# Performance work log

Measured on AMD Instinct MI355X. Metric: run time of the kernel, lower is better.

## Reference

```python
import jax, jax.numpy as jnp
import numpy as np

N_NODES = 50000
N_EDGES = 800000
HID = 128
LAYERS = 3


def setup_inputs() -> dict:
    key = jax.random.key(0)
    k1, k2, k3, k4 = jax.random.split(key, 4)
    x = jax.random.normal(k1, (N_NODES, HID), dtype=jnp.float32)
    edge_index = jax.random.randint(k2, (2, N_EDGES), 0, N_NODES, dtype=jnp.int64)
    # Glorot-ish scale so 3 stacked layers stay numerically tame
    Ws = jax.random.normal(k3, (LAYERS, HID, HID), dtype=jnp.float32) * (1.0 / np.sqrt(HID))
    bs = jax.random.normal(k4, (LAYERS, HID), dtype=jnp.float32) * 0.01
    return {"x": x, "edge_index": edge_index, "Ws": Ws, "bs": bs}


def reference(x, edge_index, Ws, bs):
    """Stacked GCNConv (add_self_loops=False): out = D^-1/2 A D^-1/2 (x W) + b.
    Returns (final_x, embeddings_list) like the torch module."""
    N = x.shape[0]
    src = edge_index[0]  # message sources (x_j)
    dst = edge_index[1]  # aggregation targets
    # gcn_norm with unit edge weights, no self loops: in-degree on targets
    deg = jax.ops.segment_sum(jnp.ones(src.shape[0], dtype=x.dtype), dst, num_segments=N)
    dinv = jnp.where(deg > 0, jax.lax.rsqrt(jnp.maximum(deg, 1.0)), 0.0).astype(x.dtype)
    norm = dinv[src] * dinv[dst]  # [E]

    embeddings = [x]
    for l in range(Ws.shape[0]):
        h = x @ Ws[l]                               # [N, D] dense transform
        msg = h[src] * norm[:, None]                # [E, D] gather + normalize
        x = jax.ops.segment_sum(msg, dst, num_segments=N) + bs[l]  # scatter-add
        embeddings.append(x)
    return (x, embeddings)
```

## Files before the change

### kernel.cpp

```cpp
#include <hip/hip_runtime.h>

#define N_NODES 50000
#define N_EDGES 800000
#define HID 128
#define SLOT (N_NODES * HID)
#define W_STRIDE (HID * HID)

#define OFF_CNT    0ul
#define OFF_DINV   200192ul
#define OFF_RPTR   400384ul
#define OFF_RFILL  600576ul
#define OFF_BSUM   800768ul
#define OFF_BOFS   801280ul
#define OFF_SRCS   801792ul
#define OFF_H_WS   4001792ul


__global__ void k_zero_cnt(int* __restrict__ cnt) {
    int i = blockIdx.x * blockDim.x + threadIdx.x;
    if (i < N_NODES) cnt[i] = 0;
}

__global__ void k_count(const int* __restrict__ ei, int* __restrict__ cnt) {
    int e = blockIdx.x * blockDim.x + threadIdx.x;
    if (e < N_EDGES) {
        int d = ei[N_EDGES + e];
        atomicAdd(&cnt[d], 1);
    }
}

__global__ void k_scan_block(const int* __restrict__ cnt, int* __restrict__ rptr,
                             int* __restrict__ bsum) {
    __shared__ int s[512];
    int tid = threadIdx.x;
    int gid = blockIdx.x * 512 + tid;
    int v = (gid < N_NODES) ? cnt[gid] : 0;
    s[tid] = v;
    __syncthreads();
    for (int off = 1; off < 512; off <<= 1) {
        int t = (tid >= off) ? s[tid - off] : 0;
        __syncthreads();
        s[tid] += t;
        __syncthreads();
    }
    if (gid < N_NODES) rptr[gid] = s[tid] - v;
    if (tid == 511) bsum[blockIdx.x] = s[511];
}

__global__ void k_scan_sums(const int* __restrict__ bsum, int* __restrict__ bofs, int nb) {
    __shared__ int s[128];
    int tid = threadIdx.x;
    int v = (tid < nb) ? bsum[tid] : 0;
    s[tid] = v;
    __syncthreads();
    for (int off = 1; off < 128; off <<= 1) {
        int t = (tid >= off) ? s[tid - off] : 0;
        __syncthreads();
        s[tid] += t;
        __syncthreads();
    }
    if (tid < nb) bofs[tid] = s[tid] - v;
}

__global__ void k_scan_add(int* __restrict__ rptr, int* __restrict__ rfill,
                           const int* __restrict__ bofs, const int* __restrict__ cnt,
                           float* __restrict__ dinv) {
    int gid = blockIdx.x * blockDim.x + threadIdx.x;
    if (gid < N_NODES) {
        int r = rptr[gid] + bofs[gid >> 9];
        rptr[gid] = r;
        rfill[gid] = r;
        int c = cnt[gid];
        dinv[gid] = (c > 0) ? rsqrtf((float)c) : 0.0f;
    }
    if (gid == 0) rptr[N_NODES] = N_EDGES;
}

__global__ void k_scatter(const int* __restrict__ ei, int* __restrict__ rfill,
                          int* __restrict__ srcs) {
    int e = blockIdx.x * blockDim.x + threadIdx.x;
    if (e < N_EDGES) {
        int sv = ei[e];
        int d  = ei[N_EDGES + e];
        int pos = atomicAdd(&rfill[d], 1);
        srcs[pos] = sv;
    }
}

__launch_bounds__(256, 2)
__global__ void k_gemm_scale(const float* __restrict__ X, const float* __restrict__ W,
                             const float* __restrict__ dinv, float* __restrict__ H) {
    __shared__ float sW[HID * 64];
    __shared__ float sX[64 * HID];
    int tid   = threadIdx.x;
    int chalf = blockIdx.x & 1;
    int row0  = (blockIdx.x >> 1) * 64;

    const float4* W4  = (const float4*)W;
    float4*       sW4 = (float4*)sW;
    for (int j = tid; j < 2048; j += 256) {
        int k  = j >> 4;
        int c4 = j & 15;
        sW4[j] = W4[k * 32 + chalf * 16 + c4];
    }

    const float4* X4  = (const float4*)X;
    float4*       sX4 = (float4*)sX;
    for (int j = tid; j < 2048; j += 256) {
        int r   = j >> 5;
        int c4  = j & 31;
        int row = row0 + r;
        float4 v = {0.f, 0.f, 0.f, 0.f};
        if (row < N_NODES) v = X4[row * 32 + c4];
        sX4[r * 32 + (c4 ^ ((r >> 3) & 7))] = v;
    }
    __syncthreads();

    int ty  = tid >> 4;
    int tx  = tid & 15;
    int swz = (ty >> 1) & 7;

    float4 acc[4];
    #pragma unroll
    for (int r = 0; r < 4; ++r) acc[r] = {0.f, 0.f, 0.f, 0.f};

    #pragma unroll 4
    for (int k0 = 0; k0 < HID; k0 += 4) {
        int k4 = k0 >> 2;
        float4 wv[4];
        #pragma unroll
        for (int kk = 0; kk < 4; ++kk)
            wv[kk] = sW4[(k0 + kk) * 16 + tx];
        float4 xv[4];
        #pragma unroll
        for (int r = 0; r < 4; ++r)
            xv[r] = sX4[(ty * 4 + r) * 32 + (k4 ^ swz)];
        #pragma unroll
        for (int r = 0; r < 4; ++r) {
            float xk0 = xv[r].x, xk1 = xv[r].y, xk2 = xv[r].z, xk3 = xv[r].w;
            acc[r].x += xk0 * wv[0].x + xk1 * wv[1].x + xk2 * wv[2].x + xk3 * wv[3].x;
            acc[r].y += xk0 * wv[0].y + xk1 * wv[1].y + xk2 * wv[2].y + xk3 * wv[3].y;
            acc[r].z += xk0 * wv[0].z + xk1 * wv[1].z + xk2 * wv[2].z + xk3 * wv[3].z;
            acc[r].w += xk0 * wv[0].w + xk1 * wv[1].w + xk2 * wv[2].w + xk3 * wv[3].w;
        }
    }

    float4* H4 = (float4*)H;
    #pragma unroll
    for (int r = 0; r < 4; ++r) {
        int row = row0 + ty * 4 + r;
        if (row < N_NODES) {
            float dv = dinv[row];
            float4 o = acc[r];
            o.x *= dv; o.y *= dv; o.z *= dv; o.w *= dv;
            H4[row * 32 + chalf * 16 + tx] = o;
        }
    }
}

__global__ void k_agg(const float* __restrict__ H, const int* __restrict__ rptr,
                      const int* __restrict__ srcs, const float* __restrict__ dinv,
                      const float* __restrict__ bias, float* __restrict__ out0,
                      float* __restrict__ out1) {
    int wid  = (blockIdx.x * blockDim.x + threadIdx.x) >> 6;
    int lane = threadIdx.x & 63;
    if (wid >= N_NODES) return;
    int half = lane >> 5;
    int l32  = lane & 31;

    int beg = rptr[wid];
    int end = rptr[wid + 1];
    int deg = end - beg;

    const float4* H4 = (const float4*)H;

    float4 a0 = {0.f,0.f,0.f,0.f}, a1 = {0.f,0.f,0.f,0.f};
    float4 a2 = {0.f,0.f,0.f,0.f}, a3 = {0.f,0.f,0.f,0.f};

    int p = beg;
    int n8 = beg + (deg & ~7);
    for (; p < n8; p += 8) {
        int base = p + half * 4;
        int s0 = srcs[base + 0];
        int s1 = srcs[base + 1];
        int s2 = srcs[base + 2];
        int s3 = srcs[base + 3];
        float4 h0 = H4[s0 * 32 + l32];
        float4 h1 = H4[s1 * 32 + l32];
        float4 h2 = H4[s2 * 32 + l32];
        float4 h3 = H4[s3 * 32 + l32];
        a0.x += h0.x; a0.y += h0.y; a0.z += h0.z; a0.w += h0.w;
        a1.x += h1.x; a1.y += h1.y; a1.z += h1.z; a1.w += h1.w;
        a2.x += h2.x; a2.y += h2.y; a2.z += h2.z; a2.w += h2.w;
        a3.x += h3.x; a3.y += h3.y; a3.z += h3.z; a3.w += h3.w;
    }
    int rem   = deg & 7;
    int pairs = rem >> 1;
    for (int i = 0; i < pairs; ++i) {
        int e = p + 2 * i + half;
        float4 hv = H4[srcs[e] * 32 + l32];
        if (i == 0)      { a0.x += hv.x; a0.y += hv.y; a0.z += hv.z; a0.w += hv.w; }
        else if (i == 1) { a1.x += hv.x; a1.y += hv.y; a1.z += hv.z; a1.w += hv.w; }
        else             { a2.x += hv.x; a2.y += hv.y; a2.z += hv.z; a2.w += hv.w; }
    }
    if (rem & 1) {
        float4 hv = H4[srcs[end - 1] * 32 + l32];
        if (half == 0) { a3.x += hv.x; a3.y += hv.y; a3.z += hv.z; a3.w += hv.w; }
    }

    float4 s;
    s.x = a0.x + a1.x + a2.x + a3.x;
    s.y = a0.y + a1.y + a2.y + a3.y;
    s.z = a0.z + a1.z + a2.z + a3.z;
    s.w = a0.w + a1.w + a2.w + a3.w;
    s.x += __shfl_xor(s.x, 32);
    s.y += __shfl_xor(s.y, 32);
    s.z += __shfl_xor(s.z, 32);
    s.w += __shfl_xor(s.w, 32);

    if (half == 0) {
        float dv  = dinv[wid];
        float4 bb = ((const float4*)bias)[l32];
        float4 res;
        res.x = s.x * dv + bb.x;
        res.y = s.y * dv + bb.y;
        res.z = s.z * dv + bb.z;
        res.w = s.w * dv + bb.w;
        ((float4*)out0)[wid * 32 + l32] = res;
        if (out1) ((float4*)out1)[wid * 32 + l32] = res;
    }
}

__global__ void k_copy(const float* __restrict__ src, float* __restrict__ dst, int n4) {
    int i = blockIdx.x * blockDim.x + threadIdx.x;
    if (i < n4) ((float4*)dst)[i] = ((const float4*)src)[i];
}


extern "C" void kernel_launch(void* const* d_in, const int* in_sizes, int n_in,
                              void* d_out, int out_size, void* d_ws, size_t ws_size,
                              hipStream_t stream) {
    const float* x  = (const float*)d_in[0];
    const int*   ei = (const int*)d_in[1];
    const float* Ws = (const float*)d_in[2];
    const float* bs = (const float*)d_in[3];
    float* out = (float*)d_out;
    char*  ws  = (char*)d_ws;

    int*   cnt   = (int*)  (ws + OFF_CNT);
    float* dinv  = (float*)(ws + OFF_DINV);
    int*   rptr  = (int*)  (ws + OFF_RPTR);
    int*   rfill = (int*)  (ws + OFF_RFILL);
    int*   bsum  = (int*)  (ws + OFF_BSUM);
    int*   bofs  = (int*)  (ws + OFF_BOFS);
    int*   srcs  = (int*)  (ws + OFF_SRCS);

    float* slot0 = out;
    float* slot1 = out + 1l * SLOT;
    float* slot2 = out + 2l * SLOT;
    float* slot3 = out + 3l * SLOT;
    float* slot4 = out + 4l * SLOT;

    bool   h_in_ws = ws_size >= (size_t)(OFF_H_WS + (size_t)SLOT * 4);
    float* h = h_in_ws ? (float*)(ws + OFF_H_WS) : slot0;

    const int NB_NODE = (N_NODES + 255) / 256;
    const int NB_EDGE = (N_EDGES + 255) / 256;
    const int NB_SCAN = (N_NODES + 511) / 512;

    k_zero_cnt  <<<NB_NODE, 256, 0, stream>>>(cnt);
    k_count     <<<NB_EDGE, 256, 0, stream>>>(ei, cnt);
    k_scan_block<<<NB_SCAN, 512, 0, stream>>>(cnt, rptr, bsum);
    k_scan_sums <<<1, 128, 0, stream>>>(bsum, bofs, NB_SCAN);
    k_scan_add  <<<NB_NODE, 256, 0, stream>>>(rptr, rfill, bofs, cnt, dinv);
    k_scatter   <<<NB_EDGE, 256, 0, stream>>>(ei, rfill, srcs);

    k_copy<<<SLOT / 4 / 256, 256, 0, stream>>>(x, slot1, SLOT / 4);

    const int NB_GEMM = 2 * ((N_NODES + 63) / 64);
    const int NB_AGG  = (N_NODES + 3) / 4;

    k_gemm_scale<<<NB_GEMM, 256, 0, stream>>>(x, Ws + 0 * W_STRIDE, dinv, h);
    k_agg       <<<NB_AGG, 256, 0, stream>>>(h, rptr, srcs, dinv, bs + 0 * HID, slot2, nullptr);

    k_gemm_scale<<<NB_GEMM, 256, 0, stream>>>(slot2, Ws + 1 * W_STRIDE, dinv, h);
    k_agg       <<<NB_AGG, 256, 0, stream>>>(h, rptr, srcs, dinv, bs + 1 * HID, slot3, nullptr);

    k_gemm_scale<<<NB_GEMM, 256, 0, stream>>>(slot3, Ws + 2 * W_STRIDE, dinv, h);
    if (h_in_ws) {
        k_agg<<<NB_AGG, 256, 0, stream>>>(h, rptr, srcs, dinv, bs + 2 * HID, slot4, slot0);
    } else {
        k_agg<<<NB_AGG, 256, 0, stream>>>(h, rptr, srcs, dinv, bs + 2 * HID, slot4, nullptr);
        k_copy<<<SLOT / 4 / 256, 256, 0, stream>>>(slot4, slot0, SLOT / 4);
    }
}
```

Before: 399.9 us.

## Fuse CSR preprocessing and input copy into one cooperative kernel

Replaces the six preprocessing launches (zero, count, block scan, sum scan, scan add, scatter) plus the input copy with a single cooperative kernel that uses grid-wide syncs between phases. The x-to-slot1 copy overlaps with the degree counting phase. This removes per-launch overhead and idle gaps between the small kernels, at the cost of grid.sync barriers and a fixed 1024-block grid. If the cooperative launch fails, it falls back to the original multi-kernel path.

```diff
diff --git a/kernel.cpp b/kernel.cpp
--- a/kernel.cpp
+++ b/kernel.cpp
@@ -1,4 +1,7 @@
 #include <hip/hip_runtime.h>
+#include <hip/hip_cooperative_groups.h>
+
+namespace cg = cooperative_groups;
 
 #define N_NODES 50000
 #define N_EDGES 800000
@@ -11,9 +14,86 @@
 #define OFF_RPTR   400384ul
 #define OFF_RFILL  600576ul
 #define OFF_BSUM   800768ul
-#define OFF_BOFS   801280ul
-#define OFF_SRCS   801792ul
-#define OFF_H_WS   4001792ul
+#define OFF_BOFS   801792ul
+#define OFF_SRCS   802816ul
+#define OFF_H_WS   4002816ul
+
+__global__ void __launch_bounds__(256, 8)
+k_preproc(const int* __restrict__ ei, const float* __restrict__ x,
+          float* __restrict__ slot1, int* __restrict__ cnt,
+          float* __restrict__ dinv, int* __restrict__ rptr,
+          int* __restrict__ rfill, int* __restrict__ bsum,
+          int* __restrict__ bofs, int* __restrict__ srcs) {
+    cg::grid_group grid = cg::this_grid();
+    const int tid = threadIdx.x;
+    const int bid = blockIdx.x;
+    const int nb  = gridDim.x;
+    const int gstride = nb * 256;
+    const int g = bid * 256 + tid;
+    const int NCHUNK = (N_NODES + 255) / 256;
+
+    __shared__ int sc[256];
+
+    for (int i = g; i < N_NODES; i += gstride) cnt[i] = 0;
+    grid.sync();
+
+    for (int e = g; e < N_EDGES; e += gstride)
+        atomicAdd(&cnt[ei[N_EDGES + e]], 1);
+    {
+        const float4* x4  = (const float4*)x;
+        float4*       s14 = (float4*)slot1;
+        for (int i = g; i < SLOT / 4; i += gstride) s14[i] = x4[i];
+    }
+    grid.sync();
+
+    for (int c = bid; c < NCHUNK; c += nb) {
+        int idx = c * 256 + tid;
+        int v = (idx < N_NODES) ? cnt[idx] : 0;
+        sc[tid] = v;
+        __syncthreads();
+        for (int off = 1; off < 256; off <<= 1) {
+            int t = (tid >= off) ? sc[tid - off] : 0;
+            __syncthreads();
+            sc[tid] += t;
+            __syncthreads();
+        }
+        if (idx < N_NODES) rptr[idx] = sc[tid] - v;
+        if (tid == 255) bsum[c] = sc[255];
+        __syncthreads();
+    }
+    grid.sync();
+
+    if (bid == 0) {
+        int v = (tid < NCHUNK) ? bsum[tid] : 0;
+        sc[tid] = v;
+        __syncthreads();
+        for (int off = 1; off < 256; off <<= 1) {
+            int t = (tid >= off) ? sc[tid - off] : 0;
+            __syncthreads();
+            sc[tid] += t;
+            __syncthreads();
+        }
+        if (tid < NCHUNK) bofs[tid] = sc[tid] - v;
+    }
+    grid.sync();
+
+    for (int i = g; i < N_NODES; i += gstride) {
+        int r = rptr[i] + bofs[i >> 8];
+        rptr[i]  = r;
+        rfill[i] = r;
+        int c = cnt[i];
+        dinv[i] = (c > 0) ? rsqrtf((float)c) : 0.0f;
+    }
+    if (g == 0) rptr[N_NODES] = N_EDGES;
+    grid.sync();
+
+    for (int e = g; e < N_EDGES; e += gstride) {
+        int sv = ei[e];
+        int d  = ei[N_EDGES + e];
+        int pos = atomicAdd(&rfill[d], 1);
+        srcs[pos] = sv;
+    }
+}
 
 
 __global__ void k_zero_cnt(int* __restrict__ cnt) {
@@ -23,10 +103,7 @@
 
 __global__ void k_count(const int* __restrict__ ei, int* __restrict__ cnt) {
     int e = blockIdx.x * blockDim.x + threadIdx.x;
-    if (e < N_EDGES) {
-        int d = ei[N_EDGES + e];
-        atomicAdd(&cnt[d], 1);
-    }
+    if (e < N_EDGES) atomicAdd(&cnt[ei[N_EDGES + e]], 1);
 }
 
 __global__ void k_scan_block(const int* __restrict__ cnt, int* __restrict__ rptr,
@@ -85,6 +162,11 @@
         int pos = atomicAdd(&rfill[d], 1);
         srcs[pos] = sv;
     }
+}
+
+__global__ void k_copy(const float* __restrict__ src, float* __restrict__ dst, int n4) {
+    int i = blockIdx.x * blockDim.x + threadIdx.x;
+    if (i < n4) ((float4*)dst)[i] = ((const float4*)src)[i];
 }
 
 __launch_bounds__(256, 2)
@@ -231,11 +313,6 @@
     }
 }
 
-__global__ void k_copy(const float* __restrict__ src, float* __restrict__ dst, int n4) {
-    int i = blockIdx.x * blockDim.x + threadIdx.x;
-    if (i < n4) ((float4*)dst)[i] = ((const float4*)src)[i];
-}
-
 
 extern "C" void kernel_launch(void* const* d_in, const int* in_sizes, int n_in,
                               void* d_out, int out_size, void* d_ws, size_t ws_size,
@@ -264,18 +341,30 @@
     bool   h_in_ws = ws_size >= (size_t)(OFF_H_WS + (size_t)SLOT * 4);
     float* h = h_in_ws ? (float*)(ws + OFF_H_WS) : slot0;
 
-    const int NB_NODE = (N_NODES + 255) / 256;
-    const int NB_EDGE = (N_EDGES + 255) / 256;
-    const int NB_SCAN = (N_NODES + 511) / 512;
-
-    k_zero_cnt  <<<NB_NODE, 256, 0, stream>>>(cnt);
-    k_count     <<<NB_EDGE, 256, 0, stream>>>(ei, cnt);
-    k_scan_block<<<NB_SCAN, 512, 0, stream>>>(cnt, rptr, bsum);
-    k_scan_sums <<<1, 128, 0, stream>>>(bsum, bofs, NB_SCAN);
-    k_scan_add  <<<NB_NODE, 256, 0, stream>>>(rptr, rfill, bofs, cnt, dinv);
-    k_scatter   <<<NB_EDGE, 256, 0, stream>>>(ei, rfill, srcs);
-
-    k_copy<<<SLOT / 4 / 256, 256, 0, stream>>>(x, slot1, SLOT / 4);
+    {
+        const int*   ei_a    = ei;
+        const float* x_a     = x;
+        float*       slot1_a = slot1;
+        void* args[] = {(void*)&ei_a, (void*)&x_a, (void*)&slot1_a,
+                        (void*)&cnt, (void*)&dinv, (void*)&rptr, (void*)&rfill,
+                        (void*)&bsum, (void*)&bofs, (void*)&srcs};
+        hipError_t err = hipLaunchCooperativeKernel((void*)k_preproc,
+                                                    dim3(1024), dim3(256),
+                                                    args, 0, stream);
+        if (err != hipSuccess) {
+            (void)hipGetLastError();
+            const int NB_NODE = (N_NODES + 255) / 256;
+            const int NB_EDGE = (N_EDGES + 255) / 256;
+            const int NB_SCAN = (N_NODES + 511) / 512;
+            k_zero_cnt  <<<NB_NODE, 256, 0, stream>>>(cnt);
+            k_count     <<<NB_EDGE, 256, 0, stream>>>(ei, cnt);
+            k_scan_block<<<NB_SCAN, 512, 0, stream>>>(cnt, rptr, bsum);
+            k_scan_sums <<<1, 128, 0, stream>>>(bsum, bofs, NB_SCAN);
+            k_scan_add  <<<NB_NODE, 256, 0, stream>>>(rptr, rfill, bofs, cnt, dinv);
+            k_scatter   <<<NB_EDGE, 256, 0, stream>>>(ei, rfill, srcs);
+            k_copy      <<<SLOT / 4 / 256, 256, 0, stream>>>(x, slot1, SLOT / 4);
+        }
+    }
 
     const int NB_GEMM = 2 * ((N_NODES + 63) / 64);
     const int NB_AGG  = (N_NODES + 3) / 4;
```

Result: slower. 884.1 us (+121.1%).

## Aggregate one node per half-wave and fold input copy into edge count kernel

Applied to the files above, without the earlier changes.

The aggregation kernel now assigns one destination node to each 32-lane half-wave instead of one per full wave, dropping the cross-half shuffle reduction and the awkward remainder handling. This halves the aggregation grid and is meant to cut idle lanes on low-degree nodes. The copy of x into the embeddings output is merged into the edge-counting kernel, and the zeroing kernel is replaced by hipMemsetAsync, saving two launches. In exchange each half-wave now walks a whole neighbor list alone, which exposes more serial latency on high-degree nodes.

```diff
diff --git a/kernel.cpp b/kernel.cpp
--- a/kernel.cpp
+++ b/kernel.cpp
@@ -11,22 +11,19 @@
 #define OFF_RPTR   400384ul
 #define OFF_RFILL  600576ul
 #define OFF_BSUM   800768ul
-#define OFF_BOFS   801280ul
-#define OFF_SRCS   801792ul
-#define OFF_H_WS   4001792ul
-
-
-__global__ void k_zero_cnt(int* __restrict__ cnt) {
-    int i = blockIdx.x * blockDim.x + threadIdx.x;
-    if (i < N_NODES) cnt[i] = 0;
-}
-
-__global__ void k_count(const int* __restrict__ ei, int* __restrict__ cnt) {
-    int e = blockIdx.x * blockDim.x + threadIdx.x;
-    if (e < N_EDGES) {
-        int d = ei[N_EDGES + e];
-        atomicAdd(&cnt[d], 1);
-    }
+#define OFF_BOFS   801792ul
+#define OFF_SRCS   802816ul
+#define OFF_H_WS   4002816ul
+
+
+__global__ void k_count(const int* __restrict__ ei, int* __restrict__ cnt,
+                        const float* __restrict__ x, float* __restrict__ slot1) {
+    int g = blockIdx.x * blockDim.x + threadIdx.x;
+    if (g < N_EDGES) atomicAdd(&cnt[ei[N_EDGES + g]], 1);
+    const float4* x4  = (const float4*)x;
+    float4*       s14 = (float4*)slot1;
+    int gs = gridDim.x * blockDim.x;
+    for (int i = g; i < SLOT / 4; i += gs) s14[i] = x4[i];
 }
 
 __global__ void k_scan_block(const int* __restrict__ cnt, int* __restrict__ rptr,
@@ -85,6 +82,11 @@
         int pos = atomicAdd(&rfill[d], 1);
         srcs[pos] = sv;
     }
+}
+
+__global__ void k_copy(const float* __restrict__ src, float* __restrict__ dst, int n4) {
+    int i = blockIdx.x * blockDim.x + threadIdx.x;
+    if (i < n4) ((float4*)dst)[i] = ((const float4*)src)[i];
 }
 
 __launch_bounds__(256, 2)
@@ -162,29 +164,27 @@
                       const int* __restrict__ srcs, const float* __restrict__ dinv,
                       const float* __restrict__ bias, float* __restrict__ out0,
                       float* __restrict__ out1) {
-    int wid  = (blockIdx.x * blockDim.x + threadIdx.x) >> 6;
+    int pair = (blockIdx.x * blockDim.x + threadIdx.x) >> 6;
     int lane = threadIdx.x & 63;
+    int wid  = pair * 2 + (lane >> 5);
+    int l32  = lane & 31;
     if (wid >= N_NODES) return;
-    int half = lane >> 5;
-    int l32  = lane & 31;
 
     int beg = rptr[wid];
     int end = rptr[wid + 1];
-    int deg = end - beg;
 
     const float4* H4 = (const float4*)H;
 
     float4 a0 = {0.f,0.f,0.f,0.f}, a1 = {0.f,0.f,0.f,0.f};
     float4 a2 = {0.f,0.f,0.f,0.f}, a3 = {0.f,0.f,0.f,0.f};
 
-    int p = beg;
-    int n8 = beg + (deg & ~7);
-    for (; p < n8; p += 8) {
-        int base = p + half * 4;
-        int s0 = srcs[base + 0];
-        int s1 = srcs[base + 1];
-        int s2 = srcs[base + 2];
-        int s3 = srcs[base + 3];
+    int p  = beg;
+    int n4 = beg + ((end - beg) & ~3);
+    for (; p < n4; p += 4) {
+        int s0 = srcs[p + 0];
+        int s1 = srcs[p + 1];
+        int s2 = srcs[p + 2];
+        int s3 = srcs[p + 3];
         float4 h0 = H4[s0 * 32 + l32];
         float4 h1 = H4[s1 * 32 + l32];
         float4 h2 = H4[s2 * 32 + l32];
@@ -194,46 +194,20 @@
         a2.x += h2.x; a2.y += h2.y; a2.z += h2.z; a2.w += h2.w;
         a3.x += h3.x; a3.y += h3.y; a3.z += h3.z; a3.w += h3.w;
     }
-    int rem   = deg & 7;
-    int pairs = rem >> 1;
-    for (int i = 0; i < pairs; ++i) {
-        int e = p + 2 * i + half;
-        float4 hv = H4[srcs[e] * 32 + l32];
-        if (i == 0)      { a0.x += hv.x; a0.y += hv.y; a0.z += hv.z; a0.w += hv.w; }
-        else if (i == 1) { a1.x += hv.x; a1.y += hv.y; a1.z += hv.z; a1.w += hv.w; }
-        else             { a2.x += hv.x; a2.y += hv.y; a2.z += hv.z; a2.w += hv.w; }
-    }
-    if (rem & 1) {
-        float4 hv = H4[srcs[end - 1] * 32 + l32];
-        if (half == 0) { a3.x += hv.x; a3.y += hv.y; a3.z += hv.z; a3.w += hv.w; }
-    }
-
-    float4 s;
-    s.x = a0.x + a1.x + a2.x + a3.x;
-    s.y = a0.y + a1.y + a2.y + a3.y;
-    s.z = a0.z + a1.z + a2.z + a3.z;
-    s.w = a0.w + a1.w + a2.w + a3.w;
-    s.x += __shfl_xor(s.x, 32);
-    s.y += __shfl_xor(s.y, 32);
-    s.z += __shfl_xor(s.z, 32);
-    s.w += __shfl_xor(s.w, 32);
-
-    if (half == 0) {
-        float dv  = dinv[wid];
-        float4 bb = ((const float4*)bias)[l32];
-        float4 res;
-        res.x = s.x * dv + bb.x;
-        res.y = s.y * dv + bb.y;
-        res.z = s.z * dv + bb.z;
-        res.w = s.w * dv + bb.w;
-        ((float4*)out0)[wid * 32 + l32] = res;
-        if (out1) ((float4*)out1)[wid * 32 + l32] = res;
-    }
-}
-
-__global__ void k_copy(const float* __restrict__ src, float* __restrict__ dst, int n4) {
-    int i = blockIdx.x * blockDim.x + threadIdx.x;
-    if (i < n4) ((float4*)dst)[i] = ((const float4*)src)[i];
+    for (; p < end; ++p) {
+        float4 hv = H4[srcs[p] * 32 + l32];
+        a0.x += hv.x; a0.y += hv.y; a0.z += hv.z; a0.w += hv.w;
+    }
+
+    float dv  = dinv[wid];
+    float4 bb = ((const float4*)bias)[l32];
+    float4 res;
+    res.x = (a0.x + a1.x + a2.x + a3.x) * dv + bb.x;
+    res.y = (a0.y + a1.y + a2.y + a3.y) * dv + bb.y;
+    res.z = (a0.z + a1.z + a2.z + a3.z) * dv + bb.z;
+    res.w = (a0.w + a1.w + a2.w + a3.w) * dv + bb.w;
+    ((float4*)out0)[wid * 32 + l32] = res;
+    if (out1) ((float4*)out1)[wid * 32 + l32] = res;
 }
 
 
@@ -268,17 +242,15 @@
     const int NB_EDGE = (N_EDGES + 255) / 256;
     const int NB_SCAN = (N_NODES + 511) / 512;
 
-    k_zero_cnt  <<<NB_NODE, 256, 0, stream>>>(cnt);
-    k_count     <<<NB_EDGE, 256, 0, stream>>>(ei, cnt);
+    hipMemsetAsync(cnt, 0, N_NODES * sizeof(int), stream);
+    k_count     <<<NB_EDGE, 256, 0, stream>>>(ei, cnt, x, slot1);
     k_scan_block<<<NB_SCAN, 512, 0, stream>>>(cnt, rptr, bsum);
     k_scan_sums <<<1, 128, 0, stream>>>(bsum, bofs, NB_SCAN);
     k_scan_add  <<<NB_NODE, 256, 0, stream>>>(rptr, rfill, bofs, cnt, dinv);
     k_scatter   <<<NB_EDGE, 256, 0, stream>>>(ei, rfill, srcs);
 
-    k_copy<<<SLOT / 4 / 256, 256, 0, stream>>>(x, slot1, SLOT / 4);
-
     const int NB_GEMM = 2 * ((N_NODES + 63) / 64);
-    const int NB_AGG  = (N_NODES + 3) / 4;
+    const int NB_AGG  = (N_NODES / 2 + 3) / 4;
 
     k_gemm_scale<<<NB_GEMM, 256, 0, stream>>>(x, Ws + 0 * W_STRIDE, dinv, h);
     k_agg       <<<NB_AGG, 256, 0, stream>>>(h, rptr, srcs, dinv, bs + 0 * HID, slot2, nullptr);
```

Result: no change. 396.7 us (-0.8%).
